# Performance work log

Hardware: AMD Instinct MI355X
Metric: run time of the kernel (lower is better)

## Reference

```python
import jax, jax.numpy as jnp
import numpy as np

EPS = 1e-5

def _ln(x, g, b):
    mu = jnp.mean(x, -1, keepdims=True)
    var = jnp.mean((x - mu) ** 2, -1, keepdims=True)
    return (x - mu) / jnp.sqrt(var + EPS) * g + b

def _edge_scores(x, lat, mask, sn_g, sn_b, tn_g, tn_b, su_w, su_b, tp_w, tp_b, m1_w, m1_b, m2_w, m2_b):
    # x: [B,S,D], lat: [B,K,D] -> edges [B,S,K]
    s = _ln(x, sn_g, sn_b) @ su_w + su_b      # [B,S,E]
    t = _ln(lat, tn_g, tn_b) @ tp_w + tp_b    # [B,K,E]
    B, S, E = s.shape
    K = t.shape[1]
    s4 = jnp.broadcast_to(s[:, :, None, :], (B, S, K, E))
    t4 = jnp.broadcast_to(t[:, None, :, :], (B, S, K, E))
    pair = jnp.concatenate([s4, t4, s4 * t4], axis=-1)  # [B,S,K,3E]
    h = jax.nn.gelu(pair @ m1_w + m1_b, approximate=False)
    e = (h @ m2_w + m2_b)[..., 0]             # [B,S,K]
    e = e / (1.0 + jnp.abs(e))                # softsign
    return e * mask[:, :, None]

def setup_inputs() -> dict:
    key = jax.random.key(0)
    B, St, Si, K, D, E = 2, 2048, 1024, 64, 768, 256
    ks = iter(jax.random.split(key, 64))
    d = {}
    d['text_values'] = jax.random.normal(next(ks), (B, St, D), jnp.float32)
    d['image_values'] = jax.random.normal(next(ks), (B, Si, D), jnp.float32)
    d['latent_state_init'] = jax.random.normal(next(ks), (B, K, D), jnp.float32)
    d['latent_value_init'] = jax.random.normal(next(ks), (B, K, D), jnp.float32)
    d['text_mask'] = jnp.ones((B, St), jnp.float32)
    d['image_mask'] = jnp.ones((B, Si), jnp.float32)
    def scorer(prefix):
        d[prefix + 'sn_g'] = jnp.ones((D,), jnp.float32)
        d[prefix + 'sn_b'] = jnp.zeros((D,), jnp.float32)
        d[prefix + 'tn_g'] = jnp.ones((D,), jnp.float32)
        d[prefix + 'tn_b'] = jnp.zeros((D,), jnp.float32)
        d[prefix + 'su_w'] = jax.random.normal(next(ks), (D, E), jnp.float32) * 0.02
        d[prefix + 'su_b'] = jnp.zeros((E,), jnp.float32)
        d[prefix + 'tp_w'] = jax.random.normal(next(ks), (D, E), jnp.float32) * 0.02
        d[prefix + 'tp_b'] = jnp.zeros((E,), jnp.float32)
        d[prefix + 'm1_w'] = jax.random.normal(next(ks), (3 * E, E), jnp.float32) * 0.02
        d[prefix + 'm1_b'] = jnp.zeros((E,), jnp.float32)
        d[prefix + 'm2_w'] = jax.random.normal(next(ks), (E, 1), jnp.float32) * 0.02
        d[prefix + 'm2_b'] = jnp.zeros((1,), jnp.float32)
    scorer('t_')
    scorer('i_')
    for p in ['tsn', 'isn', 'stn', 'vn']:
        d[p + '_g'] = jnp.ones((D,), jnp.float32)
        d[p + '_b'] = jnp.zeros((D,), jnp.float32)
    d['tsp_w'] = jax.random.normal(next(ks), (D, D), jnp.float32) * 0.02
    d['tsp_b'] = jnp.zeros((D,), jnp.float32)
    d['isp_w'] = jax.random.normal(next(ks), (D, D), jnp.float32) * 0.02
    d['isp_b'] = jnp.zeros((D,), jnp.float32)
    return d

def reference(text_values, image_values, latent_state_init, latent_value_init, text_mask, image_mask,
              t_sn_g, t_sn_b, t_tn_g, t_tn_b, t_su_w, t_su_b, t_tp_w, t_tp_b, t_m1_w, t_m1_b, t_m2_w, t_m2_b,
              i_sn_g, i_sn_b, i_tn_g, i_tn_b, i_su_w, i_su_b, i_tp_w, i_tp_b, i_m1_w, i_m1_b, i_m2_w, i_m2_b,
              tsn_g, tsn_b, isn_g, isn_b, stn_g, stn_b, vn_g, vn_b, tsp_w, tsp_b, isp_w, isp_b):
    t2l = _edge_scores(text_values, latent_value_init, text_mask,
                       t_sn_g, t_sn_b, t_tn_g, t_tn_b, t_su_w, t_su_b, t_tp_w, t_tp_b, t_m1_w, t_m1_b, t_m2_w, t_m2_b)
    i2l = _edge_scores(image_values, latent_value_init, image_mask,
                       i_sn_g, i_sn_b, i_tn_g, i_tn_b, i_su_w, i_su_b, i_tp_w, i_tp_b, i_m1_w, i_m1_b, i_m2_w, i_m2_b)
    tsf = _ln(text_values, tsn_g, tsn_b) @ tsp_w + tsp_b    # [B,St,D]
    isf = _ln(image_values, isn_g, isn_b) @ isp_w + isp_b   # [B,Si,D]
    state_raw = jnp.einsum('bsk,bsd->bkd', t2l, tsf) + jnp.einsum('bsk,bsd->bkd', i2l, isf)
    value_raw = jnp.einsum('bsk,bsd->bkd', t2l, text_values) + jnp.einsum('bsk,bsd->bkd', i2l, image_values)
    latent_state = _ln(state_raw + latent_state_init, stn_g, stn_b)
    latent_value = _ln(value_raw + latent_value_init, vn_g, vn_b)
    return latent_state, latent_value, t2l, i2l
```

## Files before the change

### kernel.cpp

```cpp
#include <hip/hip_runtime.h>
#include <math.h>

#define EPS_LN 1e-5f

#define B_  2
#define ST_ 2048
#define SI_ 1024
#define K_  64
#define D_  768
#define E_  256

typedef __bf16 bf16x8 __attribute__((ext_vector_type(8)));
typedef float  f32x4  __attribute__((ext_vector_type(4)));
typedef unsigned short ushort_t;

__device__ inline ushort_t f2bf(float x) {
    unsigned int u = __float_as_uint(x);
    unsigned int r = (u + 0x7FFFu + ((u >> 16) & 1u)) >> 16;
    return (ushort_t)r;
}

__device__ inline float erf_fast(float x) {
    float ax = fabsf(x);
    float t = __builtin_amdgcn_rcpf(fmaf(0.3275911f, ax, 1.0f));
    float poly = t * (0.254829592f + t * (-0.284496736f + t * (1.421413741f +
                 t * (-1.453152027f + t * 1.061405429f))));
    float y = 1.0f - poly * __expf(-ax * ax);
    return copysignf(y, x);
}
__device__ inline float gelu_fast(float z) {
    return 0.5f * z * (1.0f + erf_fast(z * 0.70710678118654752f));
}

__global__ __launch_bounds__(256) void ln_stats_kernel(
    const float* __restrict__ xt, const float* __restrict__ xi,
    const float* __restrict__ xl, float* __restrict__ mu, float* __restrict__ rstd)
{
    int w = threadIdx.x >> 6, lane = threadIdx.x & 63;
    int row = blockIdx.x * 4 + w;
    const float* src;
    if (row < 4096) src = xt + (size_t)row * D_;
    else if (row < 6144) src = xi + (size_t)(row - 4096) * D_;
    else src = xl + (size_t)(row - 6144) * D_;
    float s = 0.f, q = 0.f;
    #pragma unroll
    for (int rep = 0; rep < 3; ++rep) {
        float4 v = *(const float4*)(src + lane * 4 + rep * 256);
        s += v.x + v.y + v.z + v.w;
        q += v.x * v.x + v.y * v.y + v.z * v.z + v.w * v.w;
    }
    #pragma unroll
    for (int off = 32; off > 0; off >>= 1) {
        s += __shfl_xor(s, off, 64);
        q += __shfl_xor(q, off, 64);
    }
    if (lane == 0) {
        float m = s / (float)D_;
        float var = q / (float)D_ - m * m;
        mu[row] = m;
        rstd[row] = rsqrtf(var + EPS_LN);
    }
}

__global__ __launch_bounds__(256) void fold_all_kernel(
    const float* b0, const float* W0, const float* w0, float* f0,
    const float* b1, const float* W1, const float* w1, float* f1,
    const float* b2, const float* W2, const float* w2, float* f2,
    const float* b3, const float* W3, const float* w3, float* f3,
    const float* b4, const float* W4, const float* w4, float* f4,
    const float* b5, const float* W5, const float* w5, float* f5)
{
    const float* blns[6] = {b0, b1, b2, b3, b4, b5};
    const float* Ws[6]   = {W0, W1, W2, W3, W4, W5};
    const float* wbs[6]  = {w0, w1, w2, w3, w4, w5};
    float* bfs[6]        = {f0, f1, f2, f3, f4, f5};
    int cfg = blockIdx.z;
    int E = (cfg >= 4) ? 768 : 256;
    if ((int)blockIdx.x * 64 >= E) return;
    const float* bln = blns[cfg];
    const float* W = Ws[cfg];
    __shared__ float red[4][64];
    int c = threadIdx.x & 63, part = threadIdx.x >> 6;
    int e = blockIdx.x * 64 + c;
    int d0 = blockIdx.y * 64;
    float s = 0.f;
    #pragma unroll
    for (int i = 0; i < 16; ++i) {
        int d = d0 + part * 16 + i;
        s += bln[d] * W[(size_t)d * E + e];
    }
    red[part][c] = s; __syncthreads();
    if (part == 0) {
        float v = red[0][c] + red[1][c] + red[2][c] + red[3][c];
        if (blockIdx.y == 0 && wbs[cfg]) v += wbs[cfg][e];
        atomicAdd(&bfs[cfg][e], v);
    }
}

__global__ __launch_bounds__(256) void tpack_kernel(
    const float* __restrict__ xt, const float* __restrict__ xi,
    const float* __restrict__ mu, const float* __restrict__ rstd,
    ushort_t* __restrict__ XrF_t, ushort_t* __restrict__ XhF_t, ushort_t* __restrict__ AF_t,
    ushort_t* __restrict__ XrF_i, ushort_t* __restrict__ XhF_i, ushort_t* __restrict__ AF_i)
{
    __shared__ float tile[64][65];
    __shared__ float mu_s[64], rs_s[64];
    int bx = blockIdx.x;
    int isImg = bx >= 64;
    const float* x = isImg ? xi : xt;
    ushort_t* XrF = isImg ? XrF_i : XrF_t;
    ushort_t* XhF = isImg ? XhF_i : XhF_t;
    ushort_t* AF  = isImg ? AF_i  : AF_t;
    int rbase = (isImg ? bx - 64 : bx) * 64;
    int statOff = isImg ? 4096 : 0;
    int d0 = blockIdx.y * 64;
    int t = threadIdx.x;
    #pragma unroll
    for (int rep = 0; rep < 4; ++rep) {
        int rl = (t >> 4) + rep * 16;
        int c4 = (t & 15) * 4;
        *(float4*)&tile[rl][c4] = *(const float4*)(x + (size_t)(rbase + rl) * D_ + d0 + c4);
    }
    if (t < 64) { mu_s[t] = mu[statOff + rbase + t]; rs_s[t] = rstd[statOff + rbase + t]; }
    __syncthreads();
    int lane = t & 63;
    #pragma unroll
    for (int rep = 0; rep < 2; ++rep) {
        int idx = t + rep * 256;
        int nt = (idx >> 6) & 3, cl = (idx >> 8) & 1;
        int kl = cl * 32 + (lane >> 4) * 8;
        int nl = nt * 16 + (lane & 15);
        ushort_t orw[8], oh[8];
        #pragma unroll
        for (int j = 0; j < 8; ++j) {
            float v = tile[kl + j][nl];
            orw[j] = f2bf(v);
            oh[j]  = f2bf((v - mu_s[kl + j]) * rs_s[kl + j]);
        }
        size_t chunk = (size_t)((rbase >> 5) + cl);
        size_t o = ((chunk * 48 + (d0 >> 4) + nt) * 64 + lane) * 8;
        *reinterpret_cast<uint4*>(XrF + o) = *reinterpret_cast<uint4*>(orw);
        *reinterpret_cast<uint4*>(XhF + o) = *reinterpret_cast<uint4*>(oh);
    }
    #pragma unroll
    for (int rep = 0; rep < 2; ++rep) {
        int idx = t + rep * 256;
        int cl = (idx >> 6) & 1, tl = idx >> 7;
        int rl = tl * 16 + (lane & 15);
        int dl = cl * 32 + (lane >> 4) * 8;
        float m = mu_s[rl], rs = rs_s[rl];
        ushort_t o8[8];
        #pragma unroll
        for (int j = 0; j < 8; ++j)
            o8[j] = f2bf((tile[rl][dl + j] - m) * rs);
        size_t o = (((size_t)(rbase >> 4) + tl) * 24 + (d0 >> 5) + cl) * 512 + lane * 8;
        *reinterpret_cast<uint4*>(AF + o) = *reinterpret_cast<uint4*>(o8);
    }
}

__global__ __launch_bounds__(256) void packB_kernel(const float* __restrict__ W,
                                                    const float* __restrict__ g,
                                                    ushort_t* __restrict__ out,
                                                    int Kd, int N) {
    int idx = blockIdx.x * 256 + threadIdx.x;
    int nTile = N >> 4;
    int total = (Kd >> 5) * nTile * 64;
    if (idx >= total) return;
    int lane = idx & 63;
    int ntile = (idx >> 6) % nTile;
    int c = idx / (64 * nTile);
    int n = ntile * 16 + (lane & 15);
    int k0 = c * 32 + (lane >> 4) * 8;
    ushort_t o[8];
    #pragma unroll
    for (int j = 0; j < 8; ++j) {
        int k = k0 + j;
        float v = W[(size_t)k * N + n];
        if (g) v *= g[k];
        o[j] = f2bf(v);
    }
    *reinterpret_cast<uint4*>(out + (size_t)idx * 8) = *reinterpret_cast<uint4*>(o);
}

__global__ __launch_bounds__(256) void sgemm_split_kernel(
    const float* A0, const float* B0, const float* rs0, const float* bias0,
    const float* mu0, const float* sd0, int so0, float* C0,
    const float* A1, const float* B1, const float* rs1, const float* bias1,
    const float* mu1, const float* sd1, int so1, float* C1,
    int nz0, int Kd, int N)
{
    int z = blockIdx.z;
    int cfg = (z >= nz0) ? 1 : 0;
    int kz = cfg ? (z - nz0) : z;
    const float* A = cfg ? A1 : A0;
    const float* Bm = cfg ? B1 : B0;
    const float* rowScale = cfg ? rs1 : rs0;
    const float* bias = cfg ? bias1 : bias0;
    const float* muA = cfg ? mu1 : mu0;
    const float* sdA = cfg ? sd1 : sd0;
    int so = cfg ? so1 : so0;
    float* C = cfg ? C1 : C0;

    __shared__ float As[16][65];
    __shared__ float Bs[16][64];
    int tx = threadIdx.x, ty = threadIdx.y;
    int tid = ty * 16 + tx;
    int row0 = blockIdx.y * 64;
    int col0 = blockIdx.x * 64;
    float acc[4][4] = {};
    int kbase = kz * 128;
    for (int k0 = kbase; k0 < kbase + 128; k0 += 16) {
        {
            int e = tid * 4;
            int r = e >> 4, kk = e & 15;
            float4 av = *(const float4*)(A + (size_t)(row0 + r) * Kd + k0 + kk);
            if (muA) {
                float m = muA[so + row0 + r], sd = sdA[so + row0 + r];
                av.x = (av.x - m) * sd; av.y = (av.y - m) * sd;
                av.z = (av.z - m) * sd; av.w = (av.w - m) * sd;
            }
            As[kk + 0][r] = av.x; As[kk + 1][r] = av.y; As[kk + 2][r] = av.z; As[kk + 3][r] = av.w;
        }
        {
            int e = tid * 4;
            int kk = e >> 6, c = e & 63;
            float4 bv = *(const float4*)(Bm + (size_t)(k0 + kk) * N + col0 + c);
            if (rowScale) {
                float sc = rowScale[k0 + kk];
                bv.x *= sc; bv.y *= sc; bv.z *= sc; bv.w *= sc;
            }
            *(float4*)&Bs[kk][c] = bv;
        }
        __syncthreads();
        #pragma unroll
        for (int kk = 0; kk < 16; ++kk) {
            float a[4], b[4];
            #pragma unroll
            for (int i = 0; i < 4; ++i) a[i] = As[kk][ty + 16 * i];
            #pragma unroll
            for (int j = 0; j < 4; ++j) b[j] = Bs[kk][tx + 16 * j];
            #pragma unroll
            for (int i = 0; i < 4; ++i)
                #pragma unroll
                for (int j = 0; j < 4; ++j)
                    acc[i][j] += a[i] * b[j];
        }
        __syncthreads();
    }
    #pragma unroll
    for (int i = 0; i < 4; ++i) {
        int r = row0 + ty + 16 * i;
        #pragma unroll
        for (int j = 0; j < 4; ++j) {
            int c = col0 + tx + 16 * j;
            float v = acc[i][j];
            if (kz == 0 && bias) v += bias[c];
            atomicAdd(&C[(size_t)r * N + c], v);
        }
    }
}

__global__ __launch_bounds__(256) void sproj_mfma_kernel(
    const ushort_t* __restrict__ AF_t, const ushort_t* __restrict__ BF_t,
    const float* __restrict__ bias_t, ushort_t* __restrict__ sF_t,
    const ushort_t* __restrict__ AF_i, const ushort_t* __restrict__ BF_i,
    const float* __restrict__ bias_i, ushort_t* __restrict__ sF_i)
{
    __shared__ __align__(16) ushort_t ls[4][32][72];
    int bx = blockIdx.x;
    int isImg = bx >= 128;
    const ushort_t* AF = isImg ? AF_i : AF_t;
    const ushort_t* BF = isImg ? BF_i : BF_t;
    const float* bias = isImg ? bias_i : bias_t;
    ushort_t* sF = isImg ? sF_i : sF_t;
    int tile0 = (isImg ? bx - 128 : bx) * 2;

    int w = threadIdx.x >> 6, lane = threadIdx.x & 63;
    int quad = lane >> 4, n16 = lane & 15;

    f32x4 acc[2][4];
    #pragma unroll
    for (int mt = 0; mt < 2; ++mt)
        #pragma unroll
        for (int nt = 0; nt < 4; ++nt)
            acc[mt][nt] = (f32x4){0.f, 0.f, 0.f, 0.f};

    for (int c = 0; c < 24; ++c) {
        bf16x8 af[2], bf[4];
        #pragma unroll
        for (int mt = 0; mt < 2; ++mt)
            af[mt] = *reinterpret_cast<const bf16x8*>(AF + ((size_t)(tile0 + mt) * 24 + c) * 512 + lane * 8);
        #pragma unroll
        for (int nt = 0; nt < 4; ++nt)
            bf[nt] = *reinterpret_cast<const bf16x8*>(BF + ((size_t)c * 16 + w * 4 + nt) * 512 + lane * 8);
        #pragma unroll
        for (int mt = 0; mt < 2; ++mt)
            #pragma unroll
            for (int nt = 0; nt < 4; ++nt)
                acc[mt][nt] = __builtin_amdgcn_mfma_f32_16x16x32_bf16(af[mt], bf[nt], acc[mt][nt], 0, 0, 0);
    }
    #pragma unroll
    for (int mt = 0; mt < 2; ++mt)
        #pragma unroll
        for (int nt = 0; nt < 4; ++nt) {
            float bv = bias[w * 64 + nt * 16 + n16];
            #pragma unroll
            for (int r = 0; r < 4; ++r)
                ls[w][mt * 16 + quad * 4 + r][nt * 16 + n16] = f2bf(acc[mt][nt][r] + bv);
        }
    __syncthreads();
    #pragma unroll
    for (int mt = 0; mt < 2; ++mt)
        #pragma unroll
        for (int h = 0; h < 2; ++h) {
            uint4 v = *reinterpret_cast<const uint4*>(&ls[w][mt * 16 + n16][h * 32 + quad * 8]);
            *reinterpret_cast<uint4*>(sF + ((size_t)(tile0 + mt) * 8 + 2 * w + h) * 512 + lane * 8) = v;
        }
}

__global__ __launch_bounds__(256) void pack_M_kernel(
    const float* __restrict__ tP_t, const float* __restrict__ W3_t,
    const float* __restrict__ W1_t, ushort_t* __restrict__ MF_t,
    const float* __restrict__ tP_i, const float* __restrict__ W3_i,
    const float* __restrict__ W1_i, ushort_t* __restrict__ MF_i)
{
    const int HALF = B_ * K_ * 16 * 8 * 64;
    int gidx = blockIdx.x * 256 + threadIdx.x;
    int isImg = gidx >= HALF;
    int idx = isImg ? gidx - HALF : gidx;
    const float* tP = isImg ? tP_i : tP_t;
    const float* W3 = isImg ? W3_i : W3_t;
    const float* W1 = isImg ? W1_i : W1_t;
    ushort_t* MF = isImg ? MF_i : MF_t;
    int lane = idx & 63;
    int kc = (idx >> 6) & 7;
    int nt = (idx >> 9) & 15;
    int bk = idx >> 13;
    int n = nt * 16 + (lane & 15);
    int e0 = kc * 32 + (lane >> 4) * 8;
    ushort_t out[8];
    #pragma unroll
    for (int j = 0; j < 8; ++j) {
        int e = e0 + j;
        float v = tP[(size_t)bk * E_ + e] * W3[(size_t)e * E_ + n] + W1[(size_t)e * E_ + n];
        out[j] = f2bf(v);
    }
    *reinterpret_cast<uint4*>(MF + (size_t)idx * 8) = *reinterpret_cast<uint4*>(out);
}

__global__ __launch_bounds__(256, 4) void cross_mfma_kernel(
    const ushort_t* __restrict__ sF_t, const ushort_t* __restrict__ MF_t,
    const float* __restrict__ c2_t, const float* __restrict__ m2w_t,
    const float* __restrict__ m2b_t, const float* __restrict__ mask_t,
    float* __restrict__ out_t, ushort_t* __restrict__ EFt, float* __restrict__ rsum_t,
    const ushort_t* __restrict__ sF_i, const ushort_t* __restrict__ MF_i,
    const float* __restrict__ c2_i, const float* __restrict__ m2w_i,
    const float* __restrict__ m2b_i, const float* __restrict__ mask_i,
    float* __restrict__ out_i, ushort_t* __restrict__ EFi, float* __restrict__ rsum_i)
{
    int bx = blockIdx.x;
    int isImg = bx >= 32;
    int S = isImg ? SI_ : ST_;
    const ushort_t* sF = isImg ? sF_i : sF_t;
    const ushort_t* MF = isImg ? MF_i : MF_t;
    const float* c2P = isImg ? c2_i : c2_t;
    const float* m2w = isImg ? m2w_i : m2w_t;
    const float* m2b = isImg ? m2b_i : m2b_t;
    const float* mask = isImg ? mask_i : mask_t;
    float* outE = isImg ? out_i : out_t;
    ushort_t* EF = isImg ? EFi : EFt;
    float* rsum = isImg ? rsum_i : rsum_t;
    int s0 = (isImg ? bx - 32 : bx) * 64;
    int k = blockIdx.y;
    int b = blockIdx.z;
    int tid = threadIdx.x;
    int w = tid >> 6, lane = tid & 63;
    int quad = lane >> 4, n16 = lane & 15;

    const ushort_t* aBase = sF + (size_t)(b * (S / 16) + (s0 >> 4)) * 4096;
    const ushort_t* bBase = MF + ((size_t)(b * K_ + k) * 16 + w * 4) * 4096;

    f32x4 acc[4][4];
    #pragma unroll
    for (int mt = 0; mt < 4; ++mt)
        #pragma unroll
        for (int nt = 0; nt < 4; ++nt)
            acc[mt][nt] = (f32x4){0.f, 0.f, 0.f, 0.f};

    #pragma unroll
    for (int kc = 0; kc < 8; ++kc) {
        bf16x8 bfr[4], af[4];
        #pragma unroll
        for (int nt = 0; nt < 4; ++nt)
            bfr[nt] = *reinterpret_cast<const bf16x8*>(bBase + (size_t)nt * 4096 + kc * 512 + lane * 8);
        #pragma unroll
        for (int mt = 0; mt < 4; ++mt)
            af[mt] = *reinterpret_cast<const bf16x8*>(aBase + (size_t)mt * 4096 + kc * 512 + lane * 8);
        #pragma unroll
        for (int mt = 0; mt < 4; ++mt)
            #pragma unroll
            for (int nt = 0; nt < 4; ++nt)
                acc[mt][nt] = __builtin_amdgcn_mfma_f32_16x16x32_bf16(af[mt], bfr[nt], acc[mt][nt], 0, 0, 0);
    }

    const float* c2v = c2P + (size_t)(b * K_ + k) * E_;
    float c2r[4], m2r[4];
    #pragma unroll
    for (int nt = 0; nt < 4; ++nt) {
        int col = w * 64 + nt * 16 + n16;
        c2r[nt] = c2v[col];
        m2r[nt] = m2w[col];
    }
    __shared__ float pPart[4][64];
    #pragma unroll
    for (int mt = 0; mt < 4; ++mt) {
        #pragma unroll
        for (int r = 0; r < 4; ++r) {
            float p = 0.f;
            #pragma unroll
            for (int nt = 0; nt < 4; ++nt) {
                float z = acc[mt][nt][r] + c2r[nt];
                p += gelu_fast(z) * m2r[nt];
            }
            p += __shfl_xor(p, 1, 64);
            p += __shfl_xor(p, 2, 64);
            p += __shfl_xor(p, 4, 64);
            p += __shfl_xor(p, 8, 64);
            if (n16 == 0) pPart[w][mt * 16 + quad * 4 + r] = p;
        }
    }
    __syncthreads();
    if (tid < 64) {
        float e = pPart[0][tid] + pPart[1][tid] + pPart[2][tid] + pPart[3][tid] + m2b[0];
        e = e / (1.0f + fabsf(e));
        int srow = s0 + tid;
        e *= mask[(size_t)b * S + srow];
        outE[((size_t)b * S + srow) * K_ + k] = e;
        int c = (b * S + srow) >> 5;
        int mt = k >> 4;
        int lp = (k & 15) + (((srow >> 3) & 3) << 4);
        EF[(((size_t)c * 4 + mt) * 64 + lp) * 8 + (srow & 7)] = f2bf(e);
        float se = e;
        #pragma unroll
        for (int off = 32; off > 0; off >>= 1) se += __shfl_xor(se, off, 64);
        if (tid == 0) atomicAdd(&rsum[b * K_ + k], se);
    }
}

__global__ __launch_bounds__(256, 2) void einsum_mfma_kernel(
    const ushort_t* __restrict__ EF_t, const ushort_t* __restrict__ XhF_t,
    const ushort_t* __restrict__ XrF_t, float* __restrict__ PtG, float* __restrict__ PtR,
    const ushort_t* __restrict__ EF_i, const ushort_t* __restrict__ XhF_i,
    const ushort_t* __restrict__ XrF_i, float* __restrict__ PiG, float* __restrict__ PiR)
{
    int bz = blockIdx.z;
    int isImg = bz >= 2;
    int b = isImg ? bz - 2 : bz;
    int S = isImg ? SI_ : ST_;
    const ushort_t* EF = isImg ? EF_i : EF_t;
    const ushort_t* XhF = isImg ? XhF_i : XhF_t;
    const ushort_t* XrF = isImg ? XrF_i : XrF_t;
    float* PG = isImg ? PiG : PtG;
    float* PR = isImg ? PiR : PtR;
    int chunksPerBlock = S / 256;

    int w = threadIdx.x >> 6, lane = threadIdx.x & 63;
    int quad = lane >> 4, n16 = lane & 15;
    int y = blockIdx.y;
    int nt0 = blockIdx.x * 16 + w * 4;
    size_t cb = (size_t)(b * S) / 32 + (size_t)y * chunksPerBlock;

    f32x4 aG[4][4], aR[4][4];
    #pragma unroll
    for (int mt = 0; mt < 4; ++mt)
        #pragma unroll
        for (int nt = 0; nt < 4; ++nt) {
            aG[mt][nt] = (f32x4){0.f, 0.f, 0.f, 0.f};
            aR[mt][nt] = (f32x4){0.f, 0.f, 0.f, 0.f};
        }

    for (int cc = 0; cc < chunksPerBlock; ++cc) {
        size_t c = cb + cc;
        bf16x8 af[4], bh[4], bx[4];
        #pragma unroll
        for (int mt = 0; mt < 4; ++mt)
            af[mt] = *reinterpret_cast<const bf16x8*>(EF + ((c * 4 + mt) * 64 + lane) * 8);
        #pragma unroll
        for (int nt = 0; nt < 4; ++nt) {
            bh[nt] = *reinterpret_cast<const bf16x8*>(XhF + ((c * 48 + nt0 + nt) * 64 + lane) * 8);
            bx[nt] = *reinterpret_cast<const bf16x8*>(XrF + ((c * 48 + nt0 + nt) * 64 + lane) * 8);
        }
        #pragma unroll
        for (int mt = 0; mt < 4; ++mt)
            #pragma unroll
            for (int nt = 0; nt < 4; ++nt) {
                aG[mt][nt] = __builtin_amdgcn_mfma_f32_16x16x32_bf16(af[mt], bh[nt], aG[mt][nt], 0, 0, 0);
                aR[mt][nt] = __builtin_amdgcn_mfma_f32_16x16x32_bf16(af[mt], bx[nt], aR[mt][nt], 0, 0, 0);
            }
    }
    #pragma unroll
    for (int mt = 0; mt < 4; ++mt)
        #pragma unroll
        for (int nt = 0; nt < 4; ++nt) {
            int d = (nt0 + nt) * 16 + n16;
            #pragma unroll
            for (int r = 0; r < 4; ++r) {
                int krow = mt * 16 + quad * 4 + r;
                size_t o = (((size_t)y * B_ + b) * K_ + krow) * D_ + d;
                PG[o] = aG[mt][nt][r];
                PR[o] = aR[mt][nt][r];
            }
        }
}

__global__ __launch_bounds__(256) void reduce_parts_kernel(
    const float* __restrict__ PtG, const float* __restrict__ PtR,
    const float* __restrict__ PiG, const float* __restrict__ PiR,
    float* __restrict__ Gt, float* __restrict__ Gi, float* __restrict__ Racc)
{
    const int BKD = B_ * K_ * D_;
    int idx = blockIdx.x * 256 + threadIdx.x;
    if (idx >= BKD) return;
    float gt = 0.f, gi = 0.f, r = 0.f;
    #pragma unroll
    for (int c = 0; c < 8; ++c) { gt += PtG[(size_t)c * BKD + idx]; r += PtR[(size_t)c * BKD + idx]; }
    #pragma unroll
    for (int c = 0; c < 8; ++c) { gi += PiG[(size_t)c * BKD + idx]; r += PiR[(size_t)c * BKD + idx]; }
    Gt[idx] = gt; Gi[idx] = gi; Racc[idx] = r;
}

__global__ __launch_bounds__(256) void final_ln_kernel(
    const float* __restrict__ stateTmp, const float* __restrict__ Racc,
    const float* __restrict__ rs_t, const float* __restrict__ rs_i,
    const float* __restrict__ b_tspf, const float* __restrict__ b_ispf,
    const float* __restrict__ state_init, const float* __restrict__ value_init,
    const float* __restrict__ stn_g, const float* __restrict__ stn_b,
    const float* __restrict__ vn_g, const float* __restrict__ vn_b,
    float* __restrict__ outState, float* __restrict__ outValue)
{
    __shared__ float pre[D_];
    __shared__ float red[256];
    int idx = blockIdx.x;
    int row = idx & 127;
    int isVal = idx >> 7;
    int tid = threadIdx.x;
    if (!isVal) {
        float rt = rs_t[row], ri = rs_i[row];
        for (int d = tid; d < D_; d += 256)
            pre[d] = stateTmp[(size_t)row * D_ + d] + rt * b_tspf[d] + ri * b_ispf[d]
                   + state_init[(size_t)row * D_ + d];
    } else {
        for (int d = tid; d < D_; d += 256)
            pre[d] = Racc[(size_t)row * D_ + d] + value_init[(size_t)row * D_ + d];
    }
    __syncthreads();
    float s = 0.f;
    for (int d = tid; d < D_; d += 256) s += pre[d];
    red[tid] = s; __syncthreads();
    for (int off = 128; off > 0; off >>= 1) { if (tid < off) red[tid] += red[tid + off]; __syncthreads(); }
    float mu = red[0] / (float)D_;
    __syncthreads();
    float v = 0.f;
    for (int d = tid; d < D_; d += 256) { float t = pre[d] - mu; v += t * t; }
    red[tid] = v; __syncthreads();
    for (int off = 128; off > 0; off >>= 1) { if (tid < off) red[tid] += red[tid + off]; __syncthreads(); }
    float rstd = rsqrtf(red[0] / (float)D_ + EPS_LN);
    const float* g  = isVal ? vn_g : stn_g;
    const float* bb = isVal ? vn_b : stn_b;
    float* o = (isVal ? outValue : outState) + (size_t)row * D_;
    for (int d = tid; d < D_; d += 256) o[d] = (pre[d] - mu) * rstd * g[d] + bb[d];
}

extern "C" void kernel_launch(void* const* d_in, const int* in_sizes, int n_in,
                              void* d_out, int out_size, void* d_ws, size_t ws_size,
                              hipStream_t stream) {
    const float* text_values  = (const float*)d_in[0];
    const float* image_values = (const float*)d_in[1];
    const float* lstate_init  = (const float*)d_in[2];
    const float* lvalue_init  = (const float*)d_in[3];
    const float* text_mask    = (const float*)d_in[4];
    const float* image_mask   = (const float*)d_in[5];
    const float* t_sn_g = (const float*)d_in[6];
    const float* t_sn_b = (const float*)d_in[7];
    const float* t_tn_g = (const float*)d_in[8];
    const float* t_tn_b = (const float*)d_in[9];
    const float* t_su_w = (const float*)d_in[10];
    const float* t_su_b = (const float*)d_in[11];
    const float* t_tp_w = (const float*)d_in[12];
    const float* t_tp_b = (const float*)d_in[13];
    const float* t_m1_w = (const float*)d_in[14];
    const float* t_m1_b = (const float*)d_in[15];
    const float* t_m2_w = (const float*)d_in[16];
    const float* t_m2_b = (const float*)d_in[17];
    const float* i_sn_g = (const float*)d_in[18];
    const float* i_sn_b = (const float*)d_in[19];
    const float* i_tn_g = (const float*)d_in[20];
    const float* i_tn_b = (const float*)d_in[21];
    const float* i_su_w = (const float*)d_in[22];
    const float* i_su_b = (const float*)d_in[23];
    const float* i_tp_w = (const float*)d_in[24];
    const float* i_tp_b = (const float*)d_in[25];
    const float* i_m1_w = (const float*)d_in[26];
    const float* i_m1_b = (const float*)d_in[27];
    const float* i_m2_w = (const float*)d_in[28];
    const float* i_m2_b = (const float*)d_in[29];
    const float* tsn_g = (const float*)d_in[30];
    const float* tsn_b = (const float*)d_in[31];
    const float* isn_g = (const float*)d_in[32];
    const float* isn_b = (const float*)d_in[33];
    const float* stn_g = (const float*)d_in[34];
    const float* stn_b = (const float*)d_in[35];
    const float* vn_g  = (const float*)d_in[36];
    const float* vn_b  = (const float*)d_in[37];
    const float* tsp_w = (const float*)d_in[38];
    const float* tsp_b = (const float*)d_in[39];
    const float* isp_w = (const float*)d_in[40];
    const float* isp_b = (const float*)d_in[41];

    float* ws = (float*)d_ws;
    size_t o = 0;
    float* stats_mu = ws + o; o += 6272;
    float* stats_rs = ws + o; o += 6272;
    float* zeroBase = ws + o;
    float* b_su_t = ws + o; o += E_;
    float* b_su_i = ws + o; o += E_;
    float* b_tp_t = ws + o; o += E_;
    float* b_tp_i = ws + o; o += E_;
    float* b_tspf = ws + o; o += D_;
    float* b_ispf = ws + o; o += D_;
    float* t_t  = ws + o; o += (size_t)B_ * K_ * E_;
    float* t_i  = ws + o; o += (size_t)B_ * K_ * E_;
    float* c2_t = ws + o; o += (size_t)B_ * K_ * E_;
    float* c2_i = ws + o; o += (size_t)B_ * K_ * E_;
    float* state_tmp = ws + o; o += (size_t)B_ * K_ * D_;
    float* rs_t = ws + o; o += 128;
    float* rs_i = ws + o; o += 128;
    size_t zeroFloats = (size_t)(4 * E_ + 2 * D_ + 4 * B_ * K_ * E_ + B_ * K_ * D_ + 256);
    ushort_t* AF_t = (ushort_t*)(ws + o); o += (size_t)B_ * ST_ * D_ / 2;
    ushort_t* AF_i = (ushort_t*)(ws + o); o += (size_t)B_ * SI_ * D_ / 2;
    ushort_t* WsuF_t = (ushort_t*)(ws + o); o += (size_t)D_ * E_ / 2;
    ushort_t* WsuF_i = (ushort_t*)(ws + o); o += (size_t)D_ * E_ / 2;
    ushort_t* sF_t = (ushort_t*)(ws + o); o += (size_t)B_ * ST_ * E_ / 2;
    ushort_t* sF_i = (ushort_t*)(ws + o); o += (size_t)B_ * SI_ * E_ / 2;
    ushort_t* MF_t = (ushort_t*)(ws + o); o += (size_t)B_ * K_ * E_ * E_ / 2;
    ushort_t* MF_i = (ushort_t*)(ws + o); o += (size_t)B_ * K_ * E_ * E_ / 2;
    ushort_t* XhF_t = (ushort_t*)(ws + o); o += (size_t)B_ * ST_ * D_ / 2;
    ushort_t* XhF_i = (ushort_t*)(ws + o); o += (size_t)B_ * SI_ * D_ / 2;
    ushort_t* XrF_t = (ushort_t*)(ws + o); o += (size_t)B_ * ST_ * D_ / 2;
    ushort_t* XrF_i = (ushort_t*)(ws + o); o += (size_t)B_ * SI_ * D_ / 2;
    ushort_t* EF_t  = (ushort_t*)(ws + o); o += (size_t)B_ * ST_ * K_ / 2;
    ushort_t* EF_i  = (ushort_t*)(ws + o); o += (size_t)B_ * SI_ * K_ / 2;
    const int BKD = B_ * K_ * D_;
    float* PtG = ws + o; o += (size_t)8 * BKD;
    float* PtR = ws + o; o += (size_t)8 * BKD;
    float* PiG = ws + o; o += (size_t)8 * BKD;
    float* PiR = ws + o; o += (size_t)8 * BKD;
    float* Gt   = ws + o; o += BKD;
    float* Gi   = ws + o; o += BKD;
    float* Racc = ws + o; o += BKD;

    float* outState = (float*)d_out;
    float* outValue = (float*)d_out + (size_t)B_ * K_ * D_;
    float* t2l = (float*)d_out + 2 * (size_t)B_ * K_ * D_;
    float* i2l = t2l + (size_t)B_ * ST_ * K_;

    hipMemsetAsync(zeroBase, 0, zeroFloats * sizeof(float), stream);

    ln_stats_kernel<<<1568, 256, 0, stream>>>(text_values, image_values, lvalue_init, stats_mu, stats_rs);

    fold_all_kernel<<<dim3(12, 12, 6), 256, 0, stream>>>(
        t_sn_b, t_su_w, t_su_b, b_su_t,
        i_sn_b, i_su_w, i_su_b, b_su_i,
        t_tn_b, t_tp_w, t_tp_b, b_tp_t,
        i_tn_b, i_tp_w, i_tp_b, b_tp_i,
        tsn_b, tsp_w, tsp_b, b_tspf,
        isn_b, isp_w, isp_b, b_ispf);

    tpack_kernel<<<dim3(96, 12), 256, 0, stream>>>(
        text_values, image_values, stats_mu, stats_rs,
        XrF_t, XhF_t, AF_t, XrF_i, XhF_i, AF_i);

    packB_kernel<<<96, 256, 0, stream>>>(t_su_w, t_sn_g, WsuF_t, D_, E_);
    packB_kernel<<<96, 256, 0, stream>>>(i_su_w, i_sn_g, WsuF_i, D_, E_);

    sgemm_split_kernel<<<dim3(4, 2, 12), dim3(16, 16), 0, stream>>>(
        lvalue_init, t_tp_w, t_tn_g, b_tp_t, stats_mu, stats_rs, 6144, t_t,
        lvalue_init, i_tp_w, i_tn_g, b_tp_i, stats_mu, stats_rs, 6144, t_i,
        6, D_, E_);
    sgemm_split_kernel<<<dim3(4, 2, 4), dim3(16, 16), 0, stream>>>(
        t_t, t_m1_w + (size_t)E_ * E_, nullptr, t_m1_b, nullptr, nullptr, 0, c2_t,
        t_i, i_m1_w + (size_t)E_ * E_, nullptr, i_m1_b, nullptr, nullptr, 0, c2_i,
        2, E_, E_);

    sproj_mfma_kernel<<<192, 256, 0, stream>>>(
        AF_t, WsuF_t, b_su_t, sF_t, AF_i, WsuF_i, b_su_i, sF_i);

    pack_M_kernel<<<8192, 256, 0, stream>>>(
        t_t, t_m1_w + 2 * (size_t)E_ * E_, t_m1_w, MF_t,
        t_i, i_m1_w + 2 * (size_t)E_ * E_, i_m1_w, MF_i);

    cross_mfma_kernel<<<dim3(48, K_, B_), 256, 0, stream>>>(
        sF_t, MF_t, c2_t, t_m2_w, t_m2_b, text_mask, t2l, EF_t, rs_t,
        sF_i, MF_i, c2_i, i_m2_w, i_m2_b, image_mask, i2l, EF_i, rs_i);

    einsum_mfma_kernel<<<dim3(3, 8, 4), 256, 0, stream>>>(
        EF_t, XhF_t, XrF_t, PtG, PtR,
        EF_i, XhF_i, XrF_i, PiG, PiR);

    reduce_parts_kernel<<<(BKD + 255) / 256, 256, 0, stream>>>(PtG, PtR, PiG, PiR, Gt, Gi, Racc);

    sgemm_split_kernel<<<dim3(12, 2, 12), dim3(16, 16), 0, stream>>>(
        Gt, tsp_w, tsn_g, nullptr, nullptr, nullptr, 0, state_tmp,
        Gi, isp_w, isn_g, nullptr, nullptr, nullptr, 0, state_tmp,
        6, D_, D_);

    final_ln_kernel<<<2 * B_ * K_, 256, 0, stream>>>(
        state_tmp, Racc, rs_t, rs_i, b_tspf, b_ispf,
        lstate_init, lvalue_init, stn_g, stn_b, vn_g, vn_b, outState, outValue);
}
```

Before: 372.9 us.

## Swap GELU to tanh form, reorder cross grid, split E packing and rowsums out

Replaces the erf-based GELU with the tanh approximation, which uses fewer instructions but changes the numerics relative to the exact-erf reference. The cross kernel grid is reordered so k varies fastest, letting blocks that share the same sF rows run together. The scattered bf16 EF writes and atomic row sums move into separate packE and rowsum kernels, which adds launches and an extra read of the edge matrix. The einsum split doubles from 8 to 16 partial slices, giving more blocks but more partial buffers to reduce.

```diff
diff --git a/kernel.cpp b/kernel.cpp
--- a/kernel.cpp
+++ b/kernel.cpp
@@ -20,16 +20,13 @@
     return (ushort_t)r;
 }
 
-__device__ inline float erf_fast(float x) {
-    float ax = fabsf(x);
-    float t = __builtin_amdgcn_rcpf(fmaf(0.3275911f, ax, 1.0f));
-    float poly = t * (0.254829592f + t * (-0.284496736f + t * (1.421413741f +
-                 t * (-1.453152027f + t * 1.061405429f))));
-    float y = 1.0f - poly * __expf(-ax * ax);
-    return copysignf(y, x);
-}
 __device__ inline float gelu_fast(float z) {
-    return 0.5f * z * (1.0f + erf_fast(z * 0.70710678118654752f));
+    float x2 = z * z;
+    float u = 0.7978845608f * z * fmaf(0.044715f, x2, 1.0f);
+    float t = __expf(-2.0f * fabsf(u));
+    float r = __builtin_amdgcn_rcpf(1.0f + t);
+    float th = fmaf(t * r, -2.0f, 1.0f);
+    return fmaf(0.5f * fabsf(z), th, 0.5f * z);
 }
 
 __global__ __launch_bounds__(256) void ln_stats_kernel(
@@ -352,14 +349,15 @@
     const ushort_t* __restrict__ sF_t, const ushort_t* __restrict__ MF_t,
     const float* __restrict__ c2_t, const float* __restrict__ m2w_t,
     const float* __restrict__ m2b_t, const float* __restrict__ mask_t,
-    float* __restrict__ out_t, ushort_t* __restrict__ EFt, float* __restrict__ rsum_t,
+    float* __restrict__ out_t,
     const ushort_t* __restrict__ sF_i, const ushort_t* __restrict__ MF_i,
     const float* __restrict__ c2_i, const float* __restrict__ m2w_i,
     const float* __restrict__ m2b_i, const float* __restrict__ mask_i,
-    float* __restrict__ out_i, ushort_t* __restrict__ EFi, float* __restrict__ rsum_i)
-{
-    int bx = blockIdx.x;
-    int isImg = bx >= 32;
+    float* __restrict__ out_i)
+{
+    int k = blockIdx.x;
+    int by = blockIdx.y;
+    int isImg = by >= 32;
     int S = isImg ? SI_ : ST_;
     const ushort_t* sF = isImg ? sF_i : sF_t;
     const ushort_t* MF = isImg ? MF_i : MF_t;
@@ -368,10 +366,7 @@
     const float* m2b = isImg ? m2b_i : m2b_t;
     const float* mask = isImg ? mask_i : mask_t;
     float* outE = isImg ? out_i : out_t;
-    ushort_t* EF = isImg ? EFi : EFt;
-    float* rsum = isImg ? rsum_i : rsum_t;
-    int s0 = (isImg ? bx - 32 : bx) * 64;
-    int k = blockIdx.y;
+    int s0 = (isImg ? by - 32 : by) * 64;
     int b = blockIdx.z;
     int tid = threadIdx.x;
     int w = tid >> 6, lane = tid & 63;
@@ -436,15 +431,48 @@
         int srow = s0 + tid;
         e *= mask[(size_t)b * S + srow];
         outE[((size_t)b * S + srow) * K_ + k] = e;
-        int c = (b * S + srow) >> 5;
-        int mt = k >> 4;
-        int lp = (k & 15) + (((srow >> 3) & 3) << 4);
-        EF[(((size_t)c * 4 + mt) * 64 + lp) * 8 + (srow & 7)] = f2bf(e);
-        float se = e;
-        #pragma unroll
-        for (int off = 32; off > 0; off >>= 1) se += __shfl_xor(se, off, 64);
-        if (tid == 0) atomicAdd(&rsum[b * K_ + k], se);
-    }
+    }
+}
+
+__global__ __launch_bounds__(256) void packE_kernel(
+    const float* __restrict__ t2l, const float* __restrict__ i2l,
+    ushort_t* __restrict__ EF_t, ushort_t* __restrict__ EF_i)
+{
+    __shared__ float tile[32][65];
+    int g = blockIdx.x;
+    int isImg = g >= 128;
+    const float* src = isImg ? i2l : t2l;
+    ushort_t* EF = isImg ? EF_i : EF_t;
+    int chunk = isImg ? g - 128 : g;
+    int t = threadIdx.x;
+    {
+        int r = t >> 3;
+        int c4 = (t & 7) * 8;
+        const float* p = src + ((size_t)chunk * 32 + r) * 64 + c4;
+        *(float4*)&tile[r][c4] = *(const float4*)p;
+        *(float4*)&tile[r][c4 + 4] = *(const float4*)(p + 4);
+    }
+    __syncthreads();
+    int mt = t >> 6, lane = t & 63;
+    int k = mt * 16 + (lane & 15);
+    int sl0 = (lane >> 4) * 8;
+    ushort_t o8[8];
+    #pragma unroll
+    for (int j = 0; j < 8; ++j)
+        o8[j] = f2bf(tile[sl0 + j][k]);
+    *reinterpret_cast<uint4*>(EF + (((size_t)chunk * 4 + mt) * 64 + lane) * 8) = *reinterpret_cast<uint4*>(o8);
+}
+
+__global__ __launch_bounds__(256) void rowsum_kernel(const float* __restrict__ E,
+                                                     float* __restrict__ out, int S) {
+    __shared__ float red[256];
+    int idx = blockIdx.x; int b = idx >> 6; int k = idx & 63;
+    int tid = threadIdx.x;
+    float s = 0.f;
+    for (int ss = tid; ss < S; ss += 256) s += E[((size_t)b * S + ss) * K_ + k];
+    red[tid] = s; __syncthreads();
+    for (int off = 128; off > 0; off >>= 1) { if (tid < off) red[tid] += red[tid + off]; __syncthreads(); }
+    if (tid == 0) out[idx] = red[0];
 }
 
 __global__ __launch_bounds__(256, 2) void einsum_mfma_kernel(
@@ -462,7 +490,7 @@
     const ushort_t* XrF = isImg ? XrF_i : XrF_t;
     float* PG = isImg ? PiG : PtG;
     float* PR = isImg ? PiR : PtR;
-    int chunksPerBlock = S / 256;
+    int chunksPerBlock = isImg ? 2 : 4;
 
     int w = threadIdx.x >> 6, lane = threadIdx.x & 63;
     int quad = lane >> 4, n16 = lane & 15;
@@ -523,9 +551,9 @@
     if (idx >= BKD) return;
     float gt = 0.f, gi = 0.f, r = 0.f;
     #pragma unroll
-    for (int c = 0; c < 8; ++c) { gt += PtG[(size_t)c * BKD + idx]; r += PtR[(size_t)c * BKD + idx]; }
-    #pragma unroll
-    for (int c = 0; c < 8; ++c) { gi += PiG[(size_t)c * BKD + idx]; r += PiR[(size_t)c * BKD + idx]; }
+    for (int c = 0; c < 16; ++c) { gt += PtG[(size_t)c * BKD + idx]; r += PtR[(size_t)c * BKD + idx]; }
+    #pragma unroll
+    for (int c = 0; c < 16; ++c) { gi += PiG[(size_t)c * BKD + idx]; r += PiR[(size_t)c * BKD + idx]; }
     Gt[idx] = gt; Gi[idx] = gi; Racc[idx] = r;
 }
 
@@ -633,9 +661,9 @@
     float* c2_t = ws + o; o += (size_t)B_ * K_ * E_;
     float* c2_i = ws + o; o += (size_t)B_ * K_ * E_;
     float* state_tmp = ws + o; o += (size_t)B_ * K_ * D_;
+    size_t zeroFloats = (size_t)(4 * E_ + 2 * D_ + 4 * B_ * K_ * E_ + B_ * K_ * D_);
     float* rs_t = ws + o; o += 128;
     float* rs_i = ws + o; o += 128;
-    size_t zeroFloats = (size_t)(4 * E_ + 2 * D_ + 4 * B_ * K_ * E_ + B_ * K_ * D_ + 256);
     ushort_t* AF_t = (ushort_t*)(ws + o); o += (size_t)B_ * ST_ * D_ / 2;
     ushort_t* AF_i = (ushort_t*)(ws + o); o += (size_t)B_ * SI_ * D_ / 2;
     ushort_t* WsuF_t = (ushort_t*)(ws + o); o += (size_t)D_ * E_ / 2;
@@ -651,10 +679,10 @@
     ushort_t* EF_t  = (ushort_t*)(ws + o); o += (size_t)B_ * ST_ * K_ / 2;
     ushort_t* EF_i  = (ushort_t*)(ws + o); o += (size_t)B_ * SI_ * K_ / 2;
     const int BKD = B_ * K_ * D_;
-    float* PtG = ws + o; o += (size_t)8 * BKD;
-    float* PtR = ws + o; o += (size_t)8 * BKD;
-    float* PiG = ws + o; o += (size_t)8 * BKD;
-    float* PiR = ws + o; o += (size_t)8 * BKD;
+    float* PtG = ws + o; o += (size_t)16 * BKD;
+    float* PtR = ws + o; o += (size_t)16 * BKD;
+    float* PiG = ws + o; o += (size_t)16 * BKD;
+    float* PiR = ws + o; o += (size_t)16 * BKD;
     float* Gt   = ws + o; o += BKD;
     float* Gi   = ws + o; o += BKD;
     float* Racc = ws + o; o += BKD;
@@ -699,11 +727,15 @@
         t_t, t_m1_w + 2 * (size_t)E_ * E_, t_m1_w, MF_t,
         t_i, i_m1_w + 2 * (size_t)E_ * E_, i_m1_w, MF_i);
 
-    cross_mfma_kernel<<<dim3(48, K_, B_), 256, 0, stream>>>(
-        sF_t, MF_t, c2_t, t_m2_w, t_m2_b, text_mask, t2l, EF_t, rs_t,
-        sF_i, MF_i, c2_i, i_m2_w, i_m2_b, image_mask, i2l, EF_i, rs_i);
-
-    einsum_mfma_kernel<<<dim3(3, 8, 4), 256, 0, stream>>>(
+    cross_mfma_kernel<<<dim3(K_, 48, B_), 256, 0, stream>>>(
+        sF_t, MF_t, c2_t, t_m2_w, t_m2_b, text_mask, t2l,
+        sF_i, MF_i, c2_i, i_m2_w, i_m2_b, image_mask, i2l);
+
+    packE_kernel<<<192, 256, 0, stream>>>(t2l, i2l, EF_t, EF_i);
+    rowsum_kernel<<<B_ * K_, 256, 0, stream>>>(t2l, rs_t, ST_);
+    rowsum_kernel<<<B_ * K_, 256, 0, stream>>>(i2l, rs_i, SI_);
+
+    einsum_mfma_kernel<<<dim3(3, 16, 4), 256, 0, stream>>>(
         EF_t, XhF_t, XrF_t, PtG, PtR,
         EF_i, XhF_i, XrF_i, PiG, PiR);
 
```

Result: no change. 379.6 us (+1.8%).
